# Performance work log

Hardware: AMD Instinct MI355X
Metric: run time of the kernel (lower is better)

Reference implementation:

```python
import jax, jax.numpy as jnp
import numpy as np
import math

B = 512
H = 256
NHEAD = 4
DK = H // NHEAD
MAX_ATOM, MAX_PHARM, MAX_HYPER = 200, 40, 80
ATOM_CYCLE = np.array([64, 96, 128, 160, 200, 80, 120, 176])   # sum 1024 -> 65536 total
PHARM_CYCLE = np.array([8, 16, 24, 32, 12, 20, 28, 40])        # sum 180  -> 11520 total
HYPER_CYCLE = np.array([16, 32, 48, 64, 24, 40, 56, 80])       # sum 360  -> 23040 total


def _cycle_counts(cyc):
    return jnp.asarray(np.tile(cyc, B // len(cyc)), jnp.int32)


def setup_inputs() -> dict:
    key = jax.random.key(0)
    ks = jax.random.split(key, 32)
    atom_counts = _cycle_counts(ATOM_CYCLE)
    pharm_counts = _cycle_counts(PHARM_CYCLE)
    hyper_counts = _cycle_counts(HYPER_CYCLE)
    s = 1.0 / math.sqrt(H)
    lin_w = lambda k: jax.random.normal(k, (H, H), jnp.float32) * s
    lin_b = lambda k: jax.random.normal(k, (H,), jnp.float32) * 0.01
    inp = {
        'atom_message': jax.random.normal(ks[0], (int(np.tile(ATOM_CYCLE, B // 8).sum()), H), jnp.float32),
        'pharm_message': jax.random.normal(ks[1], (int(np.tile(PHARM_CYCLE, B // 8).sum()), H), jnp.float32),
        'hyper_edge_message': jax.random.normal(ks[2], (int(np.tile(HYPER_CYCLE, B // 8).sum()), H), jnp.float32),
        'atom_counts': atom_counts, 'pharm_counts': pharm_counts, 'hyper_counts': hyper_counts,
    }
    names = ['p2h_Wq', 'p2h_Wk', 'p2h_Wv', 'p2h_Wo', 'a2p_Wq', 'a2p_Wk', 'a2p_Wv', 'a2p_Wo']
    for i, n in enumerate(names):
        inp[n] = lin_w(ks[3 + i])
        inp[n.replace('W', 'b')] = lin_b(ks[11 + i])
    for d, base in enumerate(['f', 'b']):
        inp[f'gru_Wih_{base}'] = jax.random.normal(ks[19 + 4 * d], (3 * H, H), jnp.float32) * s
        inp[f'gru_Whh_{base}'] = jax.random.normal(ks[20 + 4 * d], (3 * H, H), jnp.float32) * s
        inp[f'gru_bih_{base}'] = jax.random.normal(ks[21 + 4 * d], (3 * H,), jnp.float32) * 0.01
        inp[f'gru_bhh_{base}'] = jax.random.normal(ks[22 + 4 * d], (3 * H,), jnp.float32) * 0.01
    return inp


def _pad(msg, counts, max_n):
    # vectorized equivalent of split_batch: narrow + ZeroPad2d per graph
    starts = jnp.concatenate([jnp.zeros((1,), jnp.int32), jnp.cumsum(counts)[:-1].astype(jnp.int32)])
    pos = jnp.arange(max_n)
    valid = pos[None, :] < counts[:, None]          # [B, max_n]
    idx = jnp.where(valid, starts[:, None] + pos[None, :], 0)
    return msg[idx] * valid[..., None].astype(msg.dtype)


def _mha(q, k, v, mask, Wq, bq, Wk, bk, Wv, bv, Wo, bo):
    Bn = q.shape[0]
    proj = lambda x, W, b: (x @ W.T + b).reshape(Bn, -1, NHEAD, DK).transpose(0, 2, 1, 3)
    Q, K, V = proj(q, Wq, bq), proj(k, Wk, bk), proj(v, Wv, bv)
    sc = jnp.einsum('bhqd,bhkd->bhqk', Q, K) / math.sqrt(DK)
    sc = jnp.where(mask[:, None], -1e9, sc)         # mask.unsqueeze(1) + masked_fill
    p = jax.nn.softmax(sc, axis=-1)
    x = jnp.einsum('bhqk,bhkd->bhqd', p, V).transpose(0, 2, 1, 3).reshape(Bn, -1, H)
    return x @ Wo.T + bo


def _gru_dir(x, h0, Wih, Whh, bih, bhh):
    gi = jnp.einsum('bth,gh->tbg', x, Wih) + bih    # precompute input projections, time-major
    def step(h, g):
        gh = h @ Whh.T + bhh
        ir, iz, inn = jnp.split(g, 3, -1)
        hr, hz, hn = jnp.split(gh, 3, -1)
        r = jax.nn.sigmoid(ir + hr)
        z = jax.nn.sigmoid(iz + hz)
        n = jnp.tanh(inn + r * hn)
        h2 = (1 - z) * n + z * h
        return h2, h2
    _, ys = jax.lax.scan(step, h0, gi)
    return ys.transpose(1, 0, 2)                    # back to [B, T, H]


def _forward(atom_message, pharm_message, hyper_edge_message,
             p2h_Wq, p2h_bq, p2h_Wk, p2h_bk, p2h_Wv, p2h_bv, p2h_Wo, p2h_bo,
             a2p_Wq, a2p_bq, a2p_Wk, a2p_bk, a2p_Wv, a2p_bv, a2p_Wo, a2p_bo,
             gru_Wih_f, gru_Whh_f, gru_bih_f, gru_bhh_f,
             gru_Wih_b, gru_Whh_b, gru_bih_b, gru_bhh_b,
             atom_counts, pharm_counts, hyper_counts):
    atom_f = _pad(atom_message, atom_counts, MAX_ATOM)
    pharm_f = _pad(pharm_message, pharm_counts, MAX_PHARM)
    hyper_f = _pad(hyper_edge_message, hyper_counts, MAX_HYPER)
    nz = lambda x: (x != 0).astype(jnp.float32)
    mask1 = jnp.einsum('bph,bqh->bpq', nz(pharm_f), nz(hyper_f)) == 0
    mask2 = jnp.einsum('bah,bph->bap', nz(atom_f), nz(pharm_f)) == 0
    pharm_f = _mha(pharm_f, hyper_f, hyper_f, mask1,
                   p2h_Wq, p2h_bq, p2h_Wk, p2h_bk, p2h_Wv, p2h_bv, p2h_Wo, p2h_bo) + pharm_f
    h = _mha(atom_f, pharm_f, pharm_f, mask2,
             a2p_Wq, a2p_bq, a2p_Wk, a2p_bk, a2p_Wv, a2p_bv, a2p_Wo, a2p_bo) + atom_f
    h0 = h.max(axis=1)                               # hidden init = max-pool, same for both dirs
    fwd = _gru_dir(h, h0, gru_Wih_f, gru_Whh_f, gru_bih_f, gru_bhh_f)
    bwd = _gru_dir(h[:, ::-1], h0, gru_Wih_b, gru_Whh_b, gru_bih_b, gru_bhh_b)[:, ::-1]
    h = jnp.concatenate([fwd, bwd], axis=-1)         # [B, MAX_ATOM, 2H]
    valid = (jnp.arange(MAX_ATOM)[None, :] < atom_counts[:, None]).astype(h.dtype)
    graph_embed = (h * valid[..., None]).sum(1) / atom_counts[:, None].astype(h.dtype)
    return graph_embed                               # [B, 2H]


def reference(atom_message, pharm_message, hyper_edge_message, atom_counts, pharm_counts, hyper_counts,
              p2h_Wq, p2h_bq, p2h_Wk, p2h_bk, p2h_Wv, p2h_bv, p2h_Wo, p2h_bo,
              a2p_Wq, a2p_bq, a2p_Wk, a2p_bk, a2p_Wv, a2p_bv, a2p_Wo, a2p_bo,
              gru_Wih_f, gru_Whh_f, gru_bih_f, gru_bhh_f,
              gru_Wih_b, gru_Whh_b, gru_bih_b, gru_bhh_b):
    return _forward(atom_message, pharm_message, hyper_edge_message,
                    p2h_Wq, p2h_bq, p2h_Wk, p2h_bk, p2h_Wv, p2h_bv, p2h_Wo, p2h_bo,
                    a2p_Wq, a2p_bq, a2p_Wk, a2p_bk, a2p_Wv, a2p_bv, a2p_Wo, a2p_bo,
                    gru_Wih_f, gru_Whh_f, gru_bih_f, gru_bhh_f,
                    gru_Wih_b, gru_Whh_b, gru_bih_b, gru_bhh_b,
                    atom_counts, pharm_counts, hyper_counts)
```

## Files before the change

### kernel.cpp

```cpp
#include <hip/hip_runtime.h>


typedef float f32x4 __attribute__((ext_vector_type(4)));
typedef _Float16 half8 __attribute__((ext_vector_type(8)));

#define NGRAPH 512
#define T_CH 25
#define NWIN 8
#define GI_DIR_STRIDE (512L * T_CH * 768)

#define O_SA 0L
#define O_SP 2048L
#define O_SH 4096L
#define O_WH 8192L
#define O_H0 2629632L
#define O_Q1 4194304L
#define O_K1 14680064L
#define O_V1 35651584L
#define O_Q2 4194304L
#define O_P2 56623104L
#define O_K2 67108864L
#define O_V2 77594624L
#define O_H16 56623104L
#define O_GI 4194304L
#define O_ST 43515904L

#define W_P2H_WQ 0
#define W_P2H_WK 65536
#define W_P2H_WV 131072
#define W_P2H_WO 196608
#define W_A2P_WQ 262144
#define W_A2P_WK 327680
#define W_A2P_WV 393216
#define W_A2P_WO 458752
#define W_WIH_F 524288
#define W_WHH_F 720896
#define W_WIH_B 917504
#define W_WHH_B 1114112


__global__ void prefix_k(const int* __restrict__ ca, const int* __restrict__ cp,
                         const int* __restrict__ chh,
                         int* __restrict__ sa, int* __restrict__ sp, int* __restrict__ sh) {
  __shared__ int buf[512];
  int tid = threadIdx.x;
  for (int m = 0; m < 3; ++m) {
    const int* src = (m == 0) ? ca : (m == 1) ? cp : chh;
    int* dst = (m == 0) ? sa : (m == 1) ? sp : sh;
    int v = src[tid];
    buf[tid] = v;
    __syncthreads();
    for (int off = 1; off < 512; off <<= 1) {
      int add = (tid >= off) ? buf[tid - off] : 0;
      __syncthreads();
      buf[tid] += add;
      __syncthreads();
    }
    dst[tid] = buf[tid] - v;
    __syncthreads();
  }
}

__global__ void wconv_k(const float* s0, const float* s1, const float* s2, const float* s3,
                        const float* s4, const float* s5, const float* s6, const float* s7,
                        const float* s8, const float* s9, const float* s10, const float* s11,
                        _Float16* __restrict__ dst) {
  long i = (long)blockIdx.x * 256 + threadIdx.x;
  const float* s;
  long off;
  if (i < 524288) {
    int m = (int)(i >> 16);
    off = i & 65535;
    s = (m == 0) ? s0 : (m == 1) ? s1 : (m == 2) ? s2 : (m == 3) ? s3
      : (m == 4) ? s4 : (m == 5) ? s5 : (m == 6) ? s6 : s7;
  } else {
    long r = i - 524288;
    int m = (int)(r / 196608);
    off = r - (long)m * 196608;
    s = (m == 0) ? s8 : (m == 1) ? s9 : (m == 2) ? s10 : s11;
  }
  dst[i] = (_Float16)s[off];
}

__global__ void maxpool_k(const _Float16* __restrict__ h, float* __restrict__ h0) {
  int b = blockIdx.x, j = threadIdx.x;
  float m = -1e30f;
  for (int t = 0; t < 200; ++t) m = fmaxf(m, (float)h[((long)b * 200 + t) * 256 + j]);
  h0[b * 256 + j] = m;
}

#define GF_BIAS 1
#define GF_RES  2
#define GF_GATHER 4

template <int FLAGS>
__global__ __launch_bounds__(256, 2)
void gemm_bt(const _Float16* __restrict__ A, const _Float16* __restrict__ W,
             const float* __restrict__ bias, _Float16* __restrict__ Ch,
             const float* __restrict__ rmsg, const int* __restrict__ rcnt,
             const int* __restrict__ rstart, int rmaxn, int N) {
  __shared__ _Float16 sA[128 * 40];
  __shared__ _Float16 sB[128 * 40];
  const int tid = threadIdx.x;
  const int lane = tid & 63, wave = tid >> 6;
  const int wr = wave >> 1, wc = wave & 1;
  const long bm0 = (long)blockIdx.y * 128;
  const long bn0 = (long)blockIdx.x * 128;
  const int r0 = tid >> 2, c0 = tid & 3;
  const _Float16* gB = W + (bn0 + r0) * 256 + c0 * 8;

  const _Float16* gA0 = nullptr;
  const _Float16* gA1 = nullptr;
  const float* gs0 = nullptr;
  const float* gs1 = nullptr;
  bool v0 = false, v1 = false;
  if (FLAGS & GF_GATHER) {
    int row0 = (int)bm0 + r0, row1 = row0 + 64;
    int b0 = row0 / rmaxn, p0 = row0 - b0 * rmaxn;
    int b1 = row1 / rmaxn, p1 = row1 - b1 * rmaxn;
    v0 = p0 < rcnt[b0];
    v1 = p1 < rcnt[b1];
    gs0 = rmsg + (long)(rstart[b0] + p0) * 256 + c0 * 8;
    gs1 = rmsg + (long)(rstart[b1] + p1) * 256 + c0 * 8;
  } else {
    gA0 = A + (bm0 + r0) * 256 + c0 * 8;
    gA1 = gA0 + 64 * 256;
  }
  auto loadA = [&](int kt, bool hi) -> half8 {
    if (FLAGS & GF_GATHER) {
      half8 h = {};
      const float* g = hi ? gs1 : gs0;
      if (hi ? v1 : v0) {
        float4 f0 = *(const float4*)(g + kt * 32);
        float4 f1 = *(const float4*)(g + kt * 32 + 4);
        h[0] = (_Float16)f0.x; h[1] = (_Float16)f0.y;
        h[2] = (_Float16)f0.z; h[3] = (_Float16)f0.w;
        h[4] = (_Float16)f1.x; h[5] = (_Float16)f1.y;
        h[6] = (_Float16)f1.z; h[7] = (_Float16)f1.w;
      }
      return h;
    } else {
      return hi ? *(const half8*)(gA1 + kt * 32) : *(const half8*)(gA0 + kt * 32);
    }
  };

  f32x4 acc[4][4] = {};
  half8 ra0 = loadA(0, false);
  half8 ra1 = loadA(0, true);
  half8 rb0 = *(const half8*)(gB);
  half8 rb1 = *(const half8*)(gB + 64 * 256);
  const int ar = lane & 15, kq = (lane >> 4) * 8;
  for (int kt = 0; kt < 8; ++kt) {
    __syncthreads();
    *(half8*)(sA + r0 * 40 + c0 * 8) = ra0;
    *(half8*)(sA + (r0 + 64) * 40 + c0 * 8) = ra1;
    *(half8*)(sB + r0 * 40 + c0 * 8) = rb0;
    *(half8*)(sB + (r0 + 64) * 40 + c0 * 8) = rb1;
    __syncthreads();
    if (kt < 7) {
      ra0 = loadA(kt + 1, false);
      ra1 = loadA(kt + 1, true);
      rb0 = *(const half8*)(gB + (kt + 1) * 32);
      rb1 = *(const half8*)(gB + 64 * 256 + (kt + 1) * 32);
    }
    half8 af[4], bf[4];
#pragma unroll
    for (int mt = 0; mt < 4; ++mt)
      af[mt] = *(const half8*)(sA + (wr * 64 + mt * 16 + ar) * 40 + kq);
#pragma unroll
    for (int nt = 0; nt < 4; ++nt)
      bf[nt] = *(const half8*)(sB + (wc * 64 + nt * 16 + ar) * 40 + kq);
#pragma unroll
    for (int mt = 0; mt < 4; ++mt)
#pragma unroll
      for (int nt = 0; nt < 4; ++nt)
        acc[mt][nt] = __builtin_amdgcn_mfma_f32_16x16x32_f16(af[mt], bf[nt], acc[mt][nt], 0, 0, 0);
  }
  const int cr = (lane >> 4) * 4, cc = lane & 15;
#pragma unroll
  for (int mt = 0; mt < 4; ++mt) {
#pragma unroll
    for (int nt = 0; nt < 4; ++nt) {
      const long col = bn0 + wc * 64 + nt * 16 + cc;
      float bv = (FLAGS & GF_BIAS) ? bias[col] : 0.f;
#pragma unroll
      for (int r = 0; r < 4; ++r) {
        const long row = bm0 + wr * 64 + mt * 16 + cr + r;
        float v = acc[mt][nt][r] + bv;
        if (FLAGS & GF_RES) {
          int bb = (int)(row / rmaxn);
          int p = (int)(row - (long)bb * rmaxn);
          if (p < rcnt[bb]) v += rmsg[(long)(rstart[bb] + p) * 256 + col];
        }
        Ch[row * N + col] = (_Float16)v;
      }
    }
  }
}

__global__ __launch_bounds__(256, 2)
void gemm_gi(const _Float16* __restrict__ X,
             const _Float16* __restrict__ wihf, const _Float16* __restrict__ wihb,
             _Float16* __restrict__ gi, int w) {
  __shared__ _Float16 sA[128 * 40];
  __shared__ _Float16 sB[128 * 40];
  const int dir = blockIdx.z;
  const _Float16* W = dir ? wihb : wihf;
  _Float16* Cg = gi + (long)dir * GI_DIR_STRIDE;
  const int tid = threadIdx.x;
  const int lane = tid & 63, wave = tid >> 6;
  const int wr = wave >> 1, wc = wave & 1;
  const long bm0 = (long)blockIdx.y * 128;
  const long bn0 = (long)blockIdx.x * 128;
  const int r0 = tid >> 2, c0 = tid & 3;
  int row0 = (int)bm0 + r0, row1 = row0 + 64;
  int b0 = row0 / T_CH, i0 = row0 - b0 * T_CH;
  int b1 = row1 / T_CH, i1 = row1 - b1 * T_CH;
  int t0 = dir ? (199 - T_CH * w - i0) : (T_CH * w + i0);
  int t1 = dir ? (199 - T_CH * w - i1) : (T_CH * w + i1);
  const _Float16* gA0 = X + ((long)b0 * 200 + t0) * 256 + c0 * 8;
  const _Float16* gA1 = X + ((long)b1 * 200 + t1) * 256 + c0 * 8;
  const _Float16* gB = W + (long)(bn0 + r0) * 256 + c0 * 8;

  f32x4 acc[4][4] = {};
  half8 ra0 = *(const half8*)(gA0);
  half8 ra1 = *(const half8*)(gA1);
  half8 rb0 = *(const half8*)(gB);
  half8 rb1 = *(const half8*)(gB + 64 * 256);
  const int ar = lane & 15, kq = (lane >> 4) * 8;
  for (int kt = 0; kt < 8; ++kt) {
    __syncthreads();
    *(half8*)(sA + r0 * 40 + c0 * 8) = ra0;
    *(half8*)(sA + (r0 + 64) * 40 + c0 * 8) = ra1;
    *(half8*)(sB + r0 * 40 + c0 * 8) = rb0;
    *(half8*)(sB + (r0 + 64) * 40 + c0 * 8) = rb1;
    __syncthreads();
    if (kt < 7) {
      ra0 = *(const half8*)(gA0 + (kt + 1) * 32);
      ra1 = *(const half8*)(gA1 + (kt + 1) * 32);
      rb0 = *(const half8*)(gB + (kt + 1) * 32);
      rb1 = *(const half8*)(gB + 64 * 256 + (kt + 1) * 32);
    }
    half8 af[4], bf[4];
#pragma unroll
    for (int mt = 0; mt < 4; ++mt)
      af[mt] = *(const half8*)(sA + (wr * 64 + mt * 16 + ar) * 40 + kq);
#pragma unroll
    for (int nt = 0; nt < 4; ++nt)
      bf[nt] = *(const half8*)(sB + (wc * 64 + nt * 16 + ar) * 40 + kq);
#pragma unroll
    for (int mt = 0; mt < 4; ++mt)
#pragma unroll
      for (int nt = 0; nt < 4; ++nt)
        acc[mt][nt] = __builtin_amdgcn_mfma_f32_16x16x32_f16(af[mt], bf[nt], acc[mt][nt], 0, 0, 0);
  }
  const int cr = (lane >> 4) * 4, cc = lane & 15;
#pragma unroll
  for (int mt = 0; mt < 4; ++mt)
#pragma unroll
    for (int nt = 0; nt < 4; ++nt) {
      const long col = bn0 + wc * 64 + nt * 16 + cc;
#pragma unroll
      for (int r = 0; r < 4; ++r) {
        const long row = bm0 + wr * 64 + mt * 16 + cr + r;
        Cg[row * 768 + col] = (_Float16)acc[mt][nt][r];
      }
    }
}

__global__ __launch_bounds__(256) __attribute__((amdgpu_waves_per_eu(1, 1)))
void gru_k2(const _Float16* __restrict__ gi,
            const _Float16* __restrict__ whhf, const _Float16* __restrict__ whhb,
            const float* __restrict__ bihf, const float* __restrict__ bhhf,
            const float* __restrict__ bihb, const float* __restrict__ bhhb,
            const float* __restrict__ h0, const int* __restrict__ counts,
            float* __restrict__ stateS, float* __restrict__ out, int w) {
  __shared__ _Float16 sH[16 * 264];
  __shared__ float sB[1024];
  const int blk = blockIdx.x, dir = blk >> 5, g0 = (blk & 31) << 4;
  const _Float16* Whh = dir ? whhb : whhf;
  const float* bih = dir ? bihb : bihf;
  const float* bhh = dir ? bhhb : bhhf;
  const int tid = threadIdx.x, lane = tid & 63, wave = tid >> 6;
  const int ar = lane & 15, kq = (lane >> 4) * 8;
  const int ccol = lane & 15, quad = lane >> 4;

  {
    int i = tid;
    sB[i] = bih[i] + bhh[i];
    sB[256 + i] = bih[256 + i] + bhh[256 + i];
    sB[512 + i] = bih[512 + i];
    sB[768 + i] = bhh[512 + i];
  }

  half8 wh[12][8];
#pragma unroll
  for (int g = 0; g < 3; ++g)
#pragma unroll
    for (int u = 0; u < 4; ++u) {
      const long row = (long)(g * 256 + wave * 64 + u * 16 + ar);
#pragma unroll
      for (int kt = 0; kt < 8; ++kt)
        wh[g * 4 + u][kt] = *(const half8*)(Whh + row * 256 + kt * 32 + kq);
    }

  float* st = stateS + ((long)blk * 256 + tid) * 32;
  int cn[4];
  float hs[4][4], oa[4][4];
#pragma unroll
  for (int r = 0; r < 4; ++r) cn[r] = counts[g0 + quad * 4 + r];
  if (w == 0) {
#pragma unroll
    for (int u = 0; u < 4; ++u)
#pragma unroll
      for (int r = 0; r < 4; ++r) {
        hs[u][r] = h0[(long)(g0 + quad * 4 + r) * 256 + wave * 64 + u * 16 + ccol];
        oa[u][r] = 0.f;
      }
  } else {
#pragma unroll
    for (int u = 0; u < 4; ++u)
#pragma unroll
      for (int r = 0; r < 4; ++r) {
        hs[u][r] = st[u * 4 + r];
        oa[u][r] = st[16 + u * 4 + r];
      }
  }
#pragma unroll
  for (int u = 0; u < 4; ++u)
#pragma unroll
    for (int r = 0; r < 4; ++r)
      sH[(quad * 4 + r) * 264 + wave * 64 + u * 16 + ccol] = (_Float16)hs[u][r];
  __syncthreads();

  const _Float16* gid = gi + (long)dir * GI_DIR_STRIDE;

  for (int s = 0; s < T_CH; ++s) {
    const int sg = w * T_CH + s;
    const int t = dir ? (199 - sg) : sg;
    const _Float16* gp[4];
#pragma unroll
    for (int r = 0; r < 4; ++r)
      gp[r] = gid + ((long)(g0 + quad * 4 + r) * T_CH + s) * 768 + wave * 64 + ccol;
    float gi01[2][3][4];
#pragma unroll
    for (int u = 0; u < 2; ++u)
#pragma unroll
      for (int g = 0; g < 3; ++g)
#pragma unroll
        for (int r = 0; r < 4; ++r)
          gi01[u][g][r] = (float)gp[r][g * 256 + u * 16];

    f32x4 agh[12];
#pragma unroll
    for (int i = 0; i < 12; ++i) agh[i] = (f32x4){0.f, 0.f, 0.f, 0.f};
#pragma unroll
    for (int kt = 0; kt < 8; ++kt) {
      half8 ah = *(const half8*)(sH + ar * 264 + kt * 32 + kq);
#pragma unroll
      for (int n = 0; n < 12; ++n)
        agh[n] = __builtin_amdgcn_mfma_f32_16x16x32_f16(ah, wh[n][kt], agh[n], 0, 0, 0);
    }
    __syncthreads();
    float gi23[2][3][4];
#pragma unroll
    for (int u = 0; u < 2; ++u)
#pragma unroll
      for (int g = 0; g < 3; ++g)
#pragma unroll
        for (int r = 0; r < 4; ++r)
          gi23[u][g][r] = (float)gp[r][g * 256 + (2 + u) * 16];

#pragma unroll
    for (int u = 0; u < 4; ++u) {
      const int j = wave * 64 + u * 16 + ccol;
      const float brz = sB[j];
      const float bzz = sB[256 + j];
      const float bin_ = sB[512 + j];
      const float bhn_ = sB[768 + j];
#pragma unroll
      for (int r = 0; r < 4; ++r) {
        float gir = (u < 2) ? gi01[u][0][r] : gi23[u - 2][0][r];
        float giz = (u < 2) ? gi01[u][1][r] : gi23[u - 2][1][r];
        float gin = (u < 2) ? gi01[u][2][r] : gi23[u - 2][2][r];
        float pr = agh[u][r] + gir + brz;
        float pz = agh[4 + u][r] + giz + bzz;
        float hn = agh[8 + u][r] + bhn_;
        float xn = gin + bin_;
        float rr = 1.f / (1.f + __expf(-pr));
        float zz = 1.f / (1.f + __expf(-pz));
        float e2 = __expf(2.f * (xn + rr * hn));
        float nn = 1.f - 2.f / (e2 + 1.f);
        float h2 = (1.f - zz) * nn + zz * hs[u][r];
        hs[u][r] = h2;
        if (t < cn[r]) oa[u][r] += h2;
        sH[(quad * 4 + r) * 264 + j] = (_Float16)h2;
      }
    }
    __syncthreads();
  }

  if (w == NWIN - 1) {
#pragma unroll
    for (int u = 0; u < 4; ++u)
#pragma unroll
      for (int r = 0; r < 4; ++r) {
        int j = wave * 64 + u * 16 + ccol;
        out[(long)(g0 + quad * 4 + r) * 512 + dir * 256 + j] = oa[u][r] / (float)cn[r];
      }
  } else {
#pragma unroll
    for (int u = 0; u < 4; ++u)
#pragma unroll
      for (int r = 0; r < 4; ++r) {
        st[u * 4 + r] = hs[u][r];
        st[16 + u * 4 + r] = oa[u][r];
      }
  }
}

template <int MAXQ, int MAXK, int NKP, int KKP, int CH, int SSTR, int VSTR>
__global__ __launch_bounds__(256, 2)
void mha_k(const _Float16* Qg, const _Float16* __restrict__ Kg,
           const _Float16* __restrict__ Vg, _Float16* Og,
           const int* __restrict__ qcnt, const int* __restrict__ kcnt) {
  constexpr int MTOT = (MAXQ + 15) & ~15;
  constexpr int NCH = (MTOT + CH - 1) / CH;
  __shared__ float sS[CH * SSTR];
  __shared__ _Float16 sK[NKP * 72];
  __shared__ _Float16 sV[64 * VSTR];
  const int h = blockIdx.x, b = blockIdx.y;
  const int tid = threadIdx.x, lane = tid & 63, wave = tid >> 6;
  const int qc = qcnt[b], kc = kcnt[b];
  const long qbase = ((long)b * MAXQ) * 256 + h * 64;
  const long kbase = ((long)b * MAXK) * 256 + h * 64;
  const int ar = lane & 15, kq = (lane >> 4) * 8;
  for (int i = tid; i < NKP * 64; i += 256) {
    int k = i >> 6, d = i & 63;
    sK[k * 72 + d] = (k < MAXK) ? Kg[kbase + (long)k * 256 + d] : (_Float16)0.f;
  }
  for (int i = tid; i < KKP * 64; i += 256) {
    int kk = i >> 6, d = i & 63;
    sV[d * VSTR + kk] = (kk < MAXK) ? Vg[kbase + (long)kk * 256 + d] : (_Float16)0.f;
  }
  __syncthreads();
  for (int ch = 0; ch < NCH; ++ch) {
    const int rows = (CH < MTOT - ch * CH) ? CH : (MTOT - ch * CH);
    const int mt_n = rows >> 4, st_n = NKP >> 4;
    for (int idx = wave; idx < mt_n * st_n; idx += 4) {
      int lmt = idx / st_n, nt = idx - lmt * st_n;
      int q = ch * CH + lmt * 16 + ar;
      int n0 = nt * 16;
      f32x4 acc = {0.f, 0.f, 0.f, 0.f};
#pragma unroll
      for (int ks = 0; ks < 2; ++ks) {
        half8 a = {};
        if (q < MAXQ) a = *(const half8*)(Qg + qbase + (long)q * 256 + ks * 32 + kq);
        half8 bb = *(const half8*)(sK + (n0 + ar) * 72 + ks * 32 + kq);
        acc = __builtin_amdgcn_mfma_f32_16x16x32_f16(a, bb, acc, 0, 0, 0);
      }
      int sr = lmt * 16 + (lane >> 4) * 4, sc = n0 + ar;
#pragma unroll
      for (int r = 0; r < 4; ++r) sS[(sr + r) * SSTR + sc] = acc[r];
    }
    __syncthreads();
    if (tid < rows) {
      int q = ch * CH + tid;
      float sv[MAXK];
#pragma unroll
      for (int k4 = 0; k4 < MAXK / 4; ++k4) {
        f32x4 v = *(const f32x4*)&sS[tid * SSTR + k4 * 4];
        sv[k4 * 4 + 0] = v[0]; sv[k4 * 4 + 1] = v[1];
        sv[k4 * 4 + 2] = v[2]; sv[k4 * 4 + 3] = v[3];
      }
      if (q < qc) {
        float m = -1e30f;
#pragma unroll
        for (int k = 0; k < MAXK; ++k) if (k < kc) m = fmaxf(m, sv[k]);
        float s = 0.f;
#pragma unroll
        for (int k = 0; k < MAXK; ++k) {
          float e = (k < kc) ? __expf((sv[k] - m) * 0.125f) : 0.f;
          sv[k] = e; s += e;
        }
        float inv = 1.f / s;
#pragma unroll
        for (int k = 0; k < MAXK; ++k) sv[k] *= inv;
      } else {
#pragma unroll
        for (int k = 0; k < MAXK; ++k) sv[k] = 1.f / (float)MAXK;
      }
#pragma unroll
      for (int k4 = 0; k4 < MAXK / 4; ++k4) {
        f32x4 v; v[0] = sv[k4*4+0]; v[1] = sv[k4*4+1]; v[2] = sv[k4*4+2]; v[3] = sv[k4*4+3];
        *(f32x4*)&sS[tid * SSTR + k4 * 4] = v;
      }
      for (int k = MAXK; k < KKP; ++k) sS[tid * SSTR + k] = 0.f;
    }
    __syncthreads();
    for (int idx = wave; idx < mt_n * 4; idx += 4) {
      int lmt = idx >> 2, nt = idx & 3;
      int lm = lmt * 16 + ar;
      f32x4 acc = {0.f, 0.f, 0.f, 0.f};
#pragma unroll
      for (int ks = 0; ks < KKP / 32; ++ks) {
        const float* ps = &sS[lm * SSTR + ks * 32 + kq];
        f32x4 p0 = *(const f32x4*)ps;
        f32x4 p1 = *(const f32x4*)(ps + 4);
        half8 a;
        a[0] = (_Float16)p0[0]; a[1] = (_Float16)p0[1]; a[2] = (_Float16)p0[2]; a[3] = (_Float16)p0[3];
        a[4] = (_Float16)p1[0]; a[5] = (_Float16)p1[1]; a[6] = (_Float16)p1[2]; a[7] = (_Float16)p1[3];
        half8 bb = *(const half8*)(sV + (nt * 16 + ar) * VSTR + ks * 32 + kq);
        acc = __builtin_amdgcn_mfma_f32_16x16x32_f16(a, bb, acc, 0, 0, 0);
      }
      int q0 = ch * CH + lmt * 16 + (lane >> 4) * 4;
      int dcol = nt * 16 + ar;
#pragma unroll
      for (int r = 0; r < 4; ++r) {
        int q = q0 + r;
        if (q < MAXQ) Og[qbase + (long)q * 256 + dcol] = (_Float16)acc[r];
      }
    }
    __syncthreads();
  }
}

extern "C" void kernel_launch(void* const* d_in, const int* in_sizes, int n_in,
                              void* d_out, int out_size, void* d_ws, size_t ws_size,
                              hipStream_t stream) {
  (void)in_sizes; (void)n_in; (void)out_size; (void)ws_size;
  const float* atom_msg  = (const float*)d_in[0];
  const float* pharm_msg = (const float*)d_in[1];
  const float* hyper_msg = (const float*)d_in[2];
  const int* a_cnt = (const int*)d_in[3];
  const int* p_cnt = (const int*)d_in[4];
  const int* h_cnt = (const int*)d_in[5];

  char* ws = (char*)d_ws;
  int* sa = (int*)(ws + O_SA);
  int* sp = (int*)(ws + O_SP);
  int* sh = (int*)(ws + O_SH);
  _Float16* wh = (_Float16*)(ws + O_WH);
  float* h0f = (float*)(ws + O_H0);
  _Float16* Q1 = (_Float16*)(ws + O_Q1);
  _Float16* K1 = (_Float16*)(ws + O_K1);
  _Float16* V1 = (_Float16*)(ws + O_V1);
  _Float16* Q2 = (_Float16*)(ws + O_Q2);
  _Float16* P2 = (_Float16*)(ws + O_P2);
  _Float16* K2 = (_Float16*)(ws + O_K2);
  _Float16* V2 = (_Float16*)(ws + O_V2);
  _Float16* H16 = (_Float16*)(ws + O_H16);
  _Float16* GI  = (_Float16*)(ws + O_GI);
  float* ST = (float*)(ws + O_ST);

  prefix_k<<<1, 512, 0, stream>>>(a_cnt, p_cnt, h_cnt, sa, sp, sh);
  wconv_k<<<5120, 256, 0, stream>>>(
      (const float*)d_in[6], (const float*)d_in[8], (const float*)d_in[10], (const float*)d_in[12],
      (const float*)d_in[14], (const float*)d_in[16], (const float*)d_in[18], (const float*)d_in[20],
      (const float*)d_in[22], (const float*)d_in[23], (const float*)d_in[26], (const float*)d_in[27],
      wh);

  gemm_bt<GF_BIAS | GF_GATHER><<<dim3(2, 160), 256, 0, stream>>>(nullptr, wh + W_P2H_WQ,
      (const float*)d_in[7], Q1, pharm_msg, p_cnt, sp, 40, 256);
  gemm_bt<GF_BIAS | GF_GATHER><<<dim3(2, 320), 256, 0, stream>>>(nullptr, wh + W_P2H_WK,
      (const float*)d_in[9], K1, hyper_msg, h_cnt, sh, 80, 256);
  gemm_bt<GF_BIAS | GF_GATHER><<<dim3(2, 320), 256, 0, stream>>>(nullptr, wh + W_P2H_WV,
      (const float*)d_in[11], V1, hyper_msg, h_cnt, sh, 80, 256);
  mha_k<40, 80, 80, 96, 48, 100, 104><<<dim3(4, NGRAPH), 256, 0, stream>>>(
      Q1, K1, V1, Q1, p_cnt, h_cnt);
  gemm_bt<GF_BIAS | GF_RES><<<dim3(2, 160), 256, 0, stream>>>(Q1, wh + W_P2H_WO,
      (const float*)d_in[13], P2, pharm_msg, p_cnt, sp, 40, 256);

  gemm_bt<GF_BIAS><<<dim3(2, 160), 256, 0, stream>>>(P2, wh + W_A2P_WK,
      (const float*)d_in[17], K2, nullptr, nullptr, nullptr, 1, 256);
  gemm_bt<GF_BIAS><<<dim3(2, 160), 256, 0, stream>>>(P2, wh + W_A2P_WV,
      (const float*)d_in[19], V2, nullptr, nullptr, nullptr, 1, 256);
  gemm_bt<GF_BIAS | GF_GATHER><<<dim3(2, 800), 256, 0, stream>>>(nullptr, wh + W_A2P_WQ,
      (const float*)d_in[15], Q2, atom_msg, a_cnt, sa, 200, 256);
  mha_k<200, 40, 48, 64, 112, 68, 72><<<dim3(4, NGRAPH), 256, 0, stream>>>(
      Q2, K2, V2, Q2, a_cnt, p_cnt);
  gemm_bt<GF_BIAS | GF_RES><<<dim3(2, 800), 256, 0, stream>>>(Q2, wh + W_A2P_WO,
      (const float*)d_in[21], H16, atom_msg, a_cnt, sa, 200, 256);

  maxpool_k<<<NGRAPH, 256, 0, stream>>>(H16, h0f);
  for (int w = 0; w < NWIN; ++w) {
    gemm_gi<<<dim3(6, 100, 2), 256, 0, stream>>>(H16, wh + W_WIH_F, wh + W_WIH_B, GI, w);
    gru_k2<<<64, 256, 0, stream>>>(GI, wh + W_WHH_F, wh + W_WHH_B,
        (const float*)d_in[24], (const float*)d_in[25],
        (const float*)d_in[28], (const float*)d_in[29],
        h0f, a_cnt, ST, (float*)d_out, w);
  }
}
```

Baseline: 1.911 ms.

## Split GRU recurrence across eight waves with gi-seeded MFMA accumulators

The GRU recurrent kernel now runs 512 threads (8 waves) per block, with each wave owning 32 hidden columns instead of 64. Each wave holds half as many Whh fragments in registers and issues half as many MFMAs per step. The r/z input-gate values are loaded straight into the MFMA accumulators instead of being added afterwards, and the gi pointers advance incrementally rather than being recomputed each step. The goal is to shorten the serial per-step latency of the recurrence by spreading it over more waves, at the cost of more threads taking part in each block barrier.

```diff
diff --git a/kernel.cpp b/kernel.cpp
--- a/kernel.cpp
+++ b/kernel.cpp
@@ -268,8 +268,8 @@
     }
 }
 
-__global__ __launch_bounds__(256) __attribute__((amdgpu_waves_per_eu(1, 1)))
-void gru_k2(const _Float16* __restrict__ gi,
+__global__ __launch_bounds__(512, 2)
+void gru_k3(const _Float16* __restrict__ gi,
             const _Float16* __restrict__ whhf, const _Float16* __restrict__ whhb,
             const float* __restrict__ bihf, const float* __restrict__ bhhf,
             const float* __restrict__ bihb, const float* __restrict__ bhhb,
@@ -285,7 +285,7 @@
   const int ar = lane & 15, kq = (lane >> 4) * 8;
   const int ccol = lane & 15, quad = lane >> 4;
 
-  {
+  if (tid < 256) {
     int i = tid;
     sB[i] = bih[i] + bhh[i];
     sB[256 + i] = bih[256 + i] + bhh[256 + i];
@@ -293,99 +293,89 @@
     sB[768 + i] = bhh[512 + i];
   }
 
-  half8 wh[12][8];
+  half8 wh[6][8];
 #pragma unroll
   for (int g = 0; g < 3; ++g)
 #pragma unroll
-    for (int u = 0; u < 4; ++u) {
-      const long row = (long)(g * 256 + wave * 64 + u * 16 + ar);
+    for (int u = 0; u < 2; ++u) {
+      const long row = (long)(g * 256 + wave * 32 + u * 16 + ar);
 #pragma unroll
       for (int kt = 0; kt < 8; ++kt)
-        wh[g * 4 + u][kt] = *(const half8*)(Whh + row * 256 + kt * 32 + kq);
-    }
-
-  float* st = stateS + ((long)blk * 256 + tid) * 32;
+        wh[g * 2 + u][kt] = *(const half8*)(Whh + row * 256 + kt * 32 + kq);
+    }
+
+  float* st = stateS + ((long)blk * 512 + tid) * 16;
   int cn[4];
-  float hs[4][4], oa[4][4];
+  float hs[2][4], oa[2][4];
 #pragma unroll
   for (int r = 0; r < 4; ++r) cn[r] = counts[g0 + quad * 4 + r];
   if (w == 0) {
 #pragma unroll
-    for (int u = 0; u < 4; ++u)
-#pragma unroll
-      for (int r = 0; r < 4; ++r) {
-        hs[u][r] = h0[(long)(g0 + quad * 4 + r) * 256 + wave * 64 + u * 16 + ccol];
+    for (int u = 0; u < 2; ++u)
+#pragma unroll
+      for (int r = 0; r < 4; ++r) {
+        hs[u][r] = h0[(long)(g0 + quad * 4 + r) * 256 + wave * 32 + u * 16 + ccol];
         oa[u][r] = 0.f;
       }
   } else {
 #pragma unroll
-    for (int u = 0; u < 4; ++u)
-#pragma unroll
-      for (int r = 0; r < 4; ++r) {
-        hs[u][r] = st[u * 4 + r];
-        oa[u][r] = st[16 + u * 4 + r];
-      }
-  }
-#pragma unroll
-  for (int u = 0; u < 4; ++u)
+    for (int u = 0; u < 2; ++u)
+#pragma unroll
+      for (int r = 0; r < 4; ++r) {
+        hs[u][r] = st[u * 8 + r];
+        oa[u][r] = st[u * 8 + 4 + r];
+      }
+  }
+#pragma unroll
+  for (int u = 0; u < 2; ++u)
 #pragma unroll
     for (int r = 0; r < 4; ++r)
-      sH[(quad * 4 + r) * 264 + wave * 64 + u * 16 + ccol] = (_Float16)hs[u][r];
+      sH[(quad * 4 + r) * 264 + wave * 32 + u * 16 + ccol] = (_Float16)hs[u][r];
   __syncthreads();
 
   const _Float16* gid = gi + (long)dir * GI_DIR_STRIDE;
+  const _Float16* gp[4];
+#pragma unroll
+  for (int r = 0; r < 4; ++r)
+    gp[r] = gid + ((long)(g0 + quad * 4 + r) * T_CH) * 768 + wave * 32 + ccol;
 
   for (int s = 0; s < T_CH; ++s) {
     const int sg = w * T_CH + s;
     const int t = dir ? (199 - sg) : sg;
-    const _Float16* gp[4];
-#pragma unroll
-    for (int r = 0; r < 4; ++r)
-      gp[r] = gid + ((long)(g0 + quad * 4 + r) * T_CH + s) * 768 + wave * 64 + ccol;
-    float gi01[2][3][4];
-#pragma unroll
-    for (int u = 0; u < 2; ++u)
-#pragma unroll
-      for (int g = 0; g < 3; ++g)
+    f32x4 arz[4], ahn[2];
+#pragma unroll
+    for (int g = 0; g < 2; ++g)
+#pragma unroll
+      for (int u = 0; u < 2; ++u)
 #pragma unroll
         for (int r = 0; r < 4; ++r)
-          gi01[u][g][r] = (float)gp[r][g * 256 + u * 16];
-
-    f32x4 agh[12];
-#pragma unroll
-    for (int i = 0; i < 12; ++i) agh[i] = (f32x4){0.f, 0.f, 0.f, 0.f};
+          arz[g * 2 + u][r] = (float)gp[r][g * 256 + u * 16];
+#pragma unroll
+    for (int u = 0; u < 2; ++u) ahn[u] = (f32x4){0.f, 0.f, 0.f, 0.f};
 #pragma unroll
     for (int kt = 0; kt < 8; ++kt) {
       half8 ah = *(const half8*)(sH + ar * 264 + kt * 32 + kq);
 #pragma unroll
-      for (int n = 0; n < 12; ++n)
-        agh[n] = __builtin_amdgcn_mfma_f32_16x16x32_f16(ah, wh[n][kt], agh[n], 0, 0, 0);
-    }
-    __syncthreads();
-    float gi23[2][3][4];
-#pragma unroll
-    for (int u = 0; u < 2; ++u)
-#pragma unroll
-      for (int g = 0; g < 3; ++g)
-#pragma unroll
-        for (int r = 0; r < 4; ++r)
-          gi23[u][g][r] = (float)gp[r][g * 256 + (2 + u) * 16];
-
-#pragma unroll
-    for (int u = 0; u < 4; ++u) {
-      const int j = wave * 64 + u * 16 + ccol;
+      for (int u = 0; u < 2; ++u) {
+        arz[u]     = __builtin_amdgcn_mfma_f32_16x16x32_f16(ah, wh[u][kt],     arz[u],     0, 0, 0);
+        arz[2 + u] = __builtin_amdgcn_mfma_f32_16x16x32_f16(ah, wh[2 + u][kt], arz[2 + u], 0, 0, 0);
+        ahn[u]     = __builtin_amdgcn_mfma_f32_16x16x32_f16(ah, wh[4 + u][kt], ahn[u],     0, 0, 0);
+      }
+    }
+    __syncthreads();
+#pragma unroll
+    for (int u = 0; u < 2; ++u) {
+      const int j = wave * 32 + u * 16 + ccol;
       const float brz = sB[j];
       const float bzz = sB[256 + j];
       const float bin_ = sB[512 + j];
       const float bhn_ = sB[768 + j];
 #pragma unroll
       for (int r = 0; r < 4; ++r) {
-        float gir = (u < 2) ? gi01[u][0][r] : gi23[u - 2][0][r];
-        float giz = (u < 2) ? gi01[u][1][r] : gi23[u - 2][1][r];
-        float gin = (u < 2) ? gi01[u][2][r] : gi23[u - 2][2][r];
-        float pr = agh[u][r] + gir + brz;
-        float pz = agh[4 + u][r] + giz + bzz;
-        float hn = agh[8 + u][r] + bhn_;
+        float gin = (float)gp[r][2 * 256 + u * 16];
+        float pr = arz[u][r] + brz;
+        float pz = arz[2 + u][r] + bzz;
+        float hn = ahn[u][r] + bhn_;
         float xn = gin + bin_;
         float rr = 1.f / (1.f + __expf(-pr));
         float zz = 1.f / (1.f + __expf(-pz));
@@ -397,24 +387,26 @@
         sH[(quad * 4 + r) * 264 + j] = (_Float16)h2;
       }
     }
+#pragma unroll
+    for (int r = 0; r < 4; ++r) gp[r] += 768;
     __syncthreads();
   }
 
   if (w == NWIN - 1) {
 #pragma unroll
-    for (int u = 0; u < 4; ++u)
-#pragma unroll
-      for (int r = 0; r < 4; ++r) {
-        int j = wave * 64 + u * 16 + ccol;
+    for (int u = 0; u < 2; ++u)
+#pragma unroll
+      for (int r = 0; r < 4; ++r) {
+        int j = wave * 32 + u * 16 + ccol;
         out[(long)(g0 + quad * 4 + r) * 512 + dir * 256 + j] = oa[u][r] / (float)cn[r];
       }
   } else {
 #pragma unroll
-    for (int u = 0; u < 4; ++u)
-#pragma unroll
-      for (int r = 0; r < 4; ++r) {
-        st[u * 4 + r] = hs[u][r];
-        st[16 + u * 4 + r] = oa[u][r];
+    for (int u = 0; u < 2; ++u)
+#pragma unroll
+      for (int r = 0; r < 4; ++r) {
+        st[u * 8 + r] = hs[u][r];
+        st[u * 8 + 4 + r] = oa[u][r];
       }
   }
 }
@@ -585,7 +577,7 @@
   maxpool_k<<<NGRAPH, 256, 0, stream>>>(H16, h0f);
   for (int w = 0; w < NWIN; ++w) {
     gemm_gi<<<dim3(6, 100, 2), 256, 0, stream>>>(H16, wh + W_WIH_F, wh + W_WIH_B, GI, w);
-    gru_k2<<<64, 256, 0, stream>>>(GI, wh + W_WHH_F, wh + W_WHH_B,
+    gru_k3<<<64, 512, 0, stream>>>(GI, wh + W_WHH_F, wh + W_WHH_B,
         (const float*)d_in[24], (const float*)d_in[25],
         (const float*)d_in[28], (const float*)d_in[29],
         h0f, a_cnt, ST, (float*)d_out, w);
```

Result: no change. 1.920 ms (+0.5%).
